# Kernel tuning notes

Hardware: AMD Instinct MI355X
Metric: run time of the kernel (lower is better)

Reference implementation:

```python
import jax, jax.numpy as jnp
import numpy as np

B, N, F, U = 4, 4096, 256, 128
NEG = -1.0e9


def setup_inputs() -> dict:
    key = jax.random.key(0)
    k1, k2, k3, k4, k5 = jax.random.split(key, 5)
    inputs = jax.random.normal(k1, (B, N, F), dtype=jnp.float32)
    # Glorot-normal-like scales
    w = jax.random.normal(k2, (F, U), dtype=jnp.float32) * np.sqrt(2.0 / (F + U)).astype(np.float32)
    ai = jax.random.normal(k3, (U, N), dtype=jnp.float32) * np.sqrt(2.0 / (U + N)).astype(np.float32)
    aj = jax.random.normal(k4, (U, N), dtype=jnp.float32) * np.sqrt(2.0 / (U + N)).astype(np.float32)
    a = (jax.random.uniform(k5, (N, N)) < 0.004).astype(jnp.float32)
    adj = jnp.maximum(a, a.T)
    return {"inputs": inputs, "w": w, "ai": ai, "aj": aj, "adj": adj}


def reference(inputs, w, ai, aj, adj):
    # f: [B, N, U]
    f = jnp.einsum('bnf,fu->bnu', inputs, w)
    # self_attn[b,i,j] = (f ai)[b,i,j]; other_attn = transpose([0,2,1]) of (f aj)
    self_attn = jnp.einsum('bnu,um->bnm', f, ai)          # [B, N, N]
    other_attn = jnp.einsum('bnu,um->bmn', f, aj)         # transposed [B, N, N]
    mask = adj + jnp.eye(N, dtype=adj.dtype)              # allow self + neighbors
    attn = self_attn + other_attn + NEG * (1.0 - mask)
    attn = jax.nn.softmax(attn, axis=1)                   # softmax over rows (axis=1)
    # out[b,j,u] = sum_i f[b,i,u] * attn[b,i,j]
    out = jnp.einsum('biu,bij->bju', f, attn)
    return jax.nn.relu(out), attn
```

## Files before the change

### kernel.cpp

```cpp
#include <hip/hip_runtime.h>
#include <hip/hip_bf16.h>

#define NN 4096
#define UU 128
#define BB 4
#define FF 256
#define MAXD 128

typedef float fv4 __attribute__((ext_vector_type(4)));

__device__ __forceinline__ unsigned short f2bf(float x) {
    unsigned int u = __float_as_uint(x);
    unsigned int r = (u + 0x7fffu + ((u >> 16) & 1u)) >> 16;
    return (unsigned short)r;
}
__device__ __forceinline__ float bf2f(unsigned short h) {
    return __uint_as_float(((unsigned int)h) << 16);
}

template <int CTRL, int RMASK>
__device__ __forceinline__ float dpp_step(float x) {
    int ti = __builtin_amdgcn_update_dpp(0, __float_as_int(x), CTRL, RMASK, 0xf, true);
    return x + __int_as_float(ti);
}
__device__ __forceinline__ float wave_sum_dpp(float x) {
    x = dpp_step<0x111, 0xf>(x);
    x = dpp_step<0x112, 0xf>(x);
    x = dpp_step<0x114, 0xf>(x);
    x = dpp_step<0x118, 0xf>(x);
    x = dpp_step<0x142, 0xa>(x);
    x = dpp_step<0x143, 0xc>(x);
    return __int_as_float(__builtin_amdgcn_readlane(__float_as_int(x), 63));
}

__global__ __launch_bounds__(256) void stage1(const float* __restrict__ A,
                                              const float* __restrict__ Wm,
                                              const float* __restrict__ adj,
                                              const float* __restrict__ ai,
                                              const float* __restrict__ aj,
                                              unsigned short* __restrict__ F,
                                              unsigned short* __restrict__ csc,
                                              int* __restrict__ cnt,
                                              int* __restrict__ dblf,
                                              unsigned short* __restrict__ aiT,
                                              unsigned short* __restrict__ ajT) {
    __shared__ __align__(16) char smem[21504];
    int t = threadIdx.x;
    int bid = blockIdx.x;

    if (bid < 512) {
        float (*As)[36]  = (float(*)[36])smem;
        float (*Ws)[132] = (float(*)[132])(smem + 4608);
        int r0 = bid * 32;
        int cg = t & 31;
        int rg = t >> 5;
        float acc[4][4] = {};
        for (int kc = 0; kc < FF; kc += 32) {
            {
                int row = t >> 3;
                int kb = (t & 7) * 4;
                const float* ap = A + (size_t)(r0 + row) * FF + kc + kb;
                float4 v0 = *(const float4*)(ap);
                As[kb + 0][row] = v0.x; As[kb + 1][row] = v0.y;
                As[kb + 2][row] = v0.z; As[kb + 3][row] = v0.w;
            }
#pragma unroll
            for (int q = 0; q < 4; q++) {
                int idx = q * 256 + t;
                int k = idx >> 5;
                int c4 = (idx & 31) * 4;
                *(float4*)&Ws[k][c4] = *(const float4*)(Wm + (size_t)(kc + k) * UU + c4);
            }
            __syncthreads();
#pragma unroll 8
            for (int kk = 0; kk < 32; kk++) {
                float4 a4 = *(const float4*)&As[kk][rg * 4];
                float4 w4 = *(const float4*)&Ws[kk][cg * 4];
                acc[0][0] += a4.x * w4.x; acc[0][1] += a4.x * w4.y; acc[0][2] += a4.x * w4.z; acc[0][3] += a4.x * w4.w;
                acc[1][0] += a4.y * w4.x; acc[1][1] += a4.y * w4.y; acc[1][2] += a4.y * w4.z; acc[1][3] += a4.y * w4.w;
                acc[2][0] += a4.z * w4.x; acc[2][1] += a4.z * w4.y; acc[2][2] += a4.z * w4.z; acc[2][3] += a4.z * w4.w;
                acc[3][0] += a4.w * w4.x; acc[3][1] += a4.w * w4.y; acc[3][2] += a4.w * w4.z; acc[3][3] += a4.w * w4.w;
            }
            __syncthreads();
        }
#pragma unroll
        for (int i = 0; i < 4; i++) {
            ushort4 h;
            h.x = f2bf(acc[i][0]); h.y = f2bf(acc[i][1]);
            h.z = f2bf(acc[i][2]); h.w = f2bf(acc[i][3]);
            *(ushort4*)(F + (size_t)(r0 + rg * 4 + i) * UU + cg * 4) = h;
        }
    } else if (bid < 4608) {
        unsigned short* tmp = (unsigned short*)smem;
        int* cd = (int*)(smem + 256);
        int j = bid - 512;
        if (t == 0) { cd[0] = 0; cd[1] = 0; }
        __syncthreads();
        const float4* row = (const float4*)(adj + (size_t)j * NN);
#pragma unroll
        for (int k = 0; k < 4; k++) {
            int q = t + k * 256;
            float4 v = row[q];
            int base = q * 4;
            float vals[4] = {v.x, v.y, v.z, v.w};
#pragma unroll
            for (int s = 0; s < 4; s++) {
                int i = base + s;
                bool nz = (vals[s] != 0.0f);
                if (i == j) { if (nz) cd[1] = 1; nz = true; }
                if (nz) {
                    int p = atomicAdd(&cd[0], 1);
                    if (p < MAXD) tmp[p] = (unsigned short)i;
                }
            }
        }
        __syncthreads();
        int M = cd[0] < MAXD ? cd[0] : MAXD;
        if (t < M) csc[(size_t)j * MAXD + t] = tmp[t];
        if (t == 0) { cnt[j] = M; dblf[j] = cd[1]; }
    } else {
        float (*tile)[33] = (float(*)[33])smem;
        int r = bid - 4608;
        int z = r >> 9;
        int rem = r & 511;
        int n0 = (rem >> 2) * 32;
        int u0 = (rem & 3) * 32;
        const float* src = z ? aj : ai;
        unsigned short* dst = z ? ajT : aiT;
        int tx = t & 31;
        int ty = t >> 5;
        for (int rr = 0; rr < 32; rr += 8)
            tile[ty + rr][tx] = src[(size_t)(u0 + ty + rr) * NN + n0 + tx];
        __syncthreads();
        for (int rr = 0; rr < 32; rr += 8)
            dst[(size_t)(n0 + ty + rr) * UU + u0 + tx] = f2bf(tile[tx][ty + rr]);
    }
}

__global__ __launch_bounds__(256) void gat_cols(const unsigned short* __restrict__ csc,
                                                const int* __restrict__ cnt,
                                                const int* __restrict__ dblf,
                                                const unsigned short* __restrict__ f,
                                                const unsigned short* __restrict__ aiT,
                                                const unsigned short* __restrict__ ajT,
                                                float* __restrict__ out,
                                                float* __restrict__ invden) {
    __shared__ unsigned short sidx[MAXD];
    int tid = threadIdx.x;
    int j = blockIdx.x;
    int lane = tid & 63, b = tid >> 6;
    int M = cnt[j];
    int oneh = dblf[j];
    if (tid < MAXD) sidx[tid] = csc[(size_t)j * MAXD + tid];

    const unsigned short* fb = f + (size_t)b * NN * UU;
    ushort2 fjh = *(const ushort2*)(fb + (size_t)j * UU + 2 * lane);
    float fjx = bf2f(fjh.x), fjy = bf2f(fjh.y);

    if (oneh) {
        float2 o;
        o.x = fjx > 0.0f ? fjx : 0.0f;
        o.y = fjy > 0.0f ? fjy : 0.0f;
        *(float2*)(out + ((size_t)(b * NN + j)) * UU + 2 * lane) = o;
        return;
    }
    __syncthreads();

    ushort2 aih = *(const ushort2*)(aiT + (size_t)j * UU + 2 * lane);
    float aix = bf2f(aih.x), aiy = bf2f(aih.y);
    float denom = 0.0f, acc0 = 0.0f, acc1 = 0.0f;

    int e = 0;
    for (; e + 2 <= M; e += 2) {
        int ia = sidx[e], ib2 = sidx[e + 1];
        ushort2 fha = *(const ushort2*)(fb + (size_t)ia * UU + 2 * lane);
        ushort2 aha = *(const ushort2*)(ajT + (size_t)ia * UU + 2 * lane);
        ushort2 fhb = *(const ushort2*)(fb + (size_t)ib2 * UU + 2 * lane);
        ushort2 ahb = *(const ushort2*)(ajT + (size_t)ib2 * UU + 2 * lane);
        float fax = bf2f(fha.x), fay = bf2f(fha.y);
        float fbx = bf2f(fhb.x), fby = bf2f(fhb.y);
        float pa = fax * aix + fay * aiy + fjx * bf2f(aha.x) + fjy * bf2f(aha.y);
        float pb = fbx * aix + fby * aiy + fjx * bf2f(ahb.x) + fjy * bf2f(ahb.y);
        float sa = wave_sum_dpp(pa);
        float sb = wave_sum_dpp(pb);
        float exa = __expf(sa);
        float exb = __expf(sb);
        denom += exa + exb;
        acc0 += exa * fax + exb * fbx;
        acc1 += exa * fay + exb * fby;
    }
    for (; e < M; e++) {
        int i = sidx[e];
        ushort2 fih = *(const ushort2*)(fb + (size_t)i * UU + 2 * lane);
        ushort2 ajh = *(const ushort2*)(ajT + (size_t)i * UU + 2 * lane);
        float fix = bf2f(fih.x), fiy = bf2f(fih.y);
        float p = fix * aix + fiy * aiy + fjx * bf2f(ajh.x) + fjy * bf2f(ajh.y);
        float ex = __expf(wave_sum_dpp(p));
        denom += ex;
        acc0 += ex * fix;
        acc1 += ex * fiy;
    }
    float inv = 1.0f / denom;

    float2 o;
    o.x = acc0 * inv; o.y = acc1 * inv;
    o.x = o.x > 0.0f ? o.x : 0.0f;
    o.y = o.y > 0.0f ? o.y : 0.0f;
    *(float2*)(out + ((size_t)(b * NN + j)) * UU + 2 * lane) = o;

    if (lane == 0) invden[(size_t)b * NN + j] = inv;
}

__global__ __launch_bounds__(256) void gat_rows(const unsigned short* __restrict__ csc,
                                                const int* __restrict__ cnt,
                                                const int* __restrict__ dblf,
                                                const unsigned short* __restrict__ f,
                                                const unsigned short* __restrict__ aiT,
                                                const unsigned short* __restrict__ ajT,
                                                const float* __restrict__ invden,
                                                float* __restrict__ attn) {
    __shared__ float rowv[NN];
    __shared__ unsigned short sidx[MAXD];
    int tid = threadIdx.x;
    int bi = blockIdx.x;
    int b = bi >> 12;
    int i = bi & (NN - 1);

    float4 z4 = {0.f, 0.f, 0.f, 0.f};
#pragma unroll
    for (int q = 0; q < 4; q++)
        *(float4*)&rowv[(q * 256 + tid) * 4] = z4;
    int M = cnt[i];
    if (tid < MAXD) sidx[tid] = csc[(size_t)i * MAXD + tid];
    __syncthreads();

    int lane = tid & 63, w = tid >> 6;
    const unsigned short* fb = f + (size_t)b * NN * UU;
    ushort2 fih = *(const ushort2*)(fb + (size_t)i * UU + 2 * lane);
    float fix_ = bf2f(fih.x), fiy_ = bf2f(fih.y);
    ushort2 ajh = *(const ushort2*)(ajT + (size_t)i * UU + 2 * lane);
    float ajx = bf2f(ajh.x), ajy = bf2f(ajh.y);

    for (int e = w; e < M; e += 4) {
        int j = sidx[e];
        float val;
        if (dblf[j]) {
            val = (i == j) ? 1.0f : 0.0f;
        } else {
            ushort2 fjh = *(const ushort2*)(fb + (size_t)j * UU + 2 * lane);
            ushort2 aih = *(const ushort2*)(aiT + (size_t)j * UU + 2 * lane);
            float p = fix_ * bf2f(aih.x) + fiy_ * bf2f(aih.y)
                    + bf2f(fjh.x) * ajx + bf2f(fjh.y) * ajy;
            float s = wave_sum_dpp(p);
            val = __expf(s) * invden[(size_t)b * NN + j];
        }
        if (lane == 0) rowv[j] = val;
    }
    __syncthreads();

    float* dst = attn + (size_t)bi * NN;
#pragma unroll
    for (int q = 0; q < 4; q++) {
        int c = (q * 256 + tid) * 4;
        fv4 v = *(fv4*)&rowv[c];
        __builtin_nontemporal_store(v, (fv4*)(dst + c));
    }
}

extern "C" void kernel_launch(void* const* d_in, const int* in_sizes, int n_in,
                              void* d_out, int out_size, void* d_ws, size_t ws_size,
                              hipStream_t stream) {
    const float* inputs = (const float*)d_in[0];
    const float* w      = (const float*)d_in[1];
    const float* ai     = (const float*)d_in[2];
    const float* aj     = (const float*)d_in[3];
    const float* adj    = (const float*)d_in[4];

    float* out  = (float*)d_out;
    float* attn = out + (size_t)BB * NN * UU;

    unsigned short* f   = (unsigned short*)d_ws;
    unsigned short* aiT = f + (size_t)BB * NN * UU;
    unsigned short* ajT = aiT + (size_t)NN * UU;
    unsigned short* csc = ajT + (size_t)NN * UU;
    int* cnt  = (int*)(csc + (size_t)NN * MAXD);
    int* dblf = cnt + NN;
    float* invden = (float*)(dblf + NN);

    stage1<<<5632, 256, 0, stream>>>(inputs, w, adj, ai, aj, f, csc, cnt, dblf, aiT, ajT);
    gat_cols<<<NN, 256, 0, stream>>>(csc, cnt, dblf, f, aiT, ajT, out, invden);
    gat_rows<<<BB * NN, 256, 0, stream>>>(csc, cnt, dblf, f, aiT, ajT, invden, attn);
}
```

Baseline: 387.7 us.

## Store per-edge attention weights in column pass and scatter them into rows

The column kernel now keeps each edge's exp value, scales it by the inverse denominator and writes it to a per-column buffer. A new set of blocks builds a row-to-(column, edge slot) map with atomics. The row kernel then just gathers these stored values instead of recomputing dot products, wave reductions and exps. This removes the duplicated score computation in exchange for extra workspace traffic and an atomic map-building step.

After: 413.3 us. +6.6%, slower.

```diff
diff --git a/kernel.cpp b/kernel.cpp
--- a/kernel.cpp
+++ b/kernel.cpp
@@ -43,7 +43,8 @@
                                               int* __restrict__ cnt,
                                               int* __restrict__ dblf,
                                               unsigned short* __restrict__ aiT,
-                                              unsigned short* __restrict__ ajT) {
+                                              unsigned short* __restrict__ ajT,
+                                              int* __restrict__ mcnt) {
     __shared__ __align__(16) char smem[21504];
     int t = threadIdx.x;
     int bid = blockIdx.x;
@@ -118,7 +119,7 @@
         int M = cd[0] < MAXD ? cd[0] : MAXD;
         if (t < M) csc[(size_t)j * MAXD + t] = tmp[t];
         if (t == 0) { cnt[j] = M; dblf[j] = cd[1]; }
-    } else {
+    } else if (bid < 5632) {
         float (*tile)[33] = (float(*)[33])smem;
         int r = bid - 4608;
         int z = r >> 9;
@@ -134,30 +135,54 @@
         __syncthreads();
         for (int rr = 0; rr < 32; rr += 8)
             dst[(size_t)(n0 + ty + rr) * UU + u0 + tx] = f2bf(tile[tx][ty + rr]);
-    }
-}
-
-__global__ __launch_bounds__(256) void gat_cols(const unsigned short* __restrict__ csc,
-                                                const int* __restrict__ cnt,
-                                                const int* __restrict__ dblf,
-                                                const unsigned short* __restrict__ f,
-                                                const unsigned short* __restrict__ aiT,
-                                                const unsigned short* __restrict__ ajT,
-                                                float* __restrict__ out,
-                                                float* __restrict__ invden) {
+    } else {
+        int4 z = {0, 0, 0, 0};
+#pragma unroll
+        for (int q = 0; q < 4; q++)
+            *(int4*)&mcnt[(q * 256 + t) * 4] = z;
+    }
+}
+
+__global__ __launch_bounds__(256) void stage2(const unsigned short* __restrict__ csc,
+                                              const int* __restrict__ cnt,
+                                              const int* __restrict__ dblf,
+                                              const unsigned short* __restrict__ f,
+                                              const unsigned short* __restrict__ aiT,
+                                              const unsigned short* __restrict__ ajT,
+                                              float* __restrict__ out,
+                                              float* __restrict__ tmpv,
+                                              unsigned int* __restrict__ mJE,
+                                              int* __restrict__ mcnt) {
+    int tid = threadIdx.x;
+    int bid = blockIdx.x;
+    int j = bid >> 1;
+
+    if (bid & 1) {
+        int M = cnt[j];
+        if (tid < M) {
+            int i = csc[(size_t)j * MAXD + tid];
+            int p = atomicAdd(&mcnt[i], 1);
+            mJE[(size_t)i * MAXD + p] = ((unsigned int)j << 7) | (unsigned int)tid;
+        }
+        return;
+    }
+
     __shared__ unsigned short sidx[MAXD];
-    int tid = threadIdx.x;
-    int j = blockIdx.x;
     int lane = tid & 63, b = tid >> 6;
     int M = cnt[j];
     int oneh = dblf[j];
     if (tid < MAXD) sidx[tid] = csc[(size_t)j * MAXD + tid];
 
     const unsigned short* fb = f + (size_t)b * NN * UU;
+    float* tv = tmpv + (((size_t)b << 12) + j) * MAXD;
     ushort2 fjh = *(const ushort2*)(fb + (size_t)j * UU + 2 * lane);
     float fjx = bf2f(fjh.x), fjy = bf2f(fjh.y);
 
     if (oneh) {
+        int g0 = csc[(size_t)j * MAXD + lane];
+        int g1 = csc[(size_t)j * MAXD + lane + 64];
+        if (lane < M)      tv[lane]      = (g0 == j) ? 1.0f : 0.0f;
+        if (lane + 64 < M) tv[lane + 64] = (g1 == j) ? 1.0f : 0.0f;
         float2 o;
         o.x = fjx > 0.0f ? fjx : 0.0f;
         o.y = fjy > 0.0f ? fjy : 0.0f;
@@ -169,6 +194,7 @@
     ushort2 aih = *(const ushort2*)(aiT + (size_t)j * UU + 2 * lane);
     float aix = bf2f(aih.x), aiy = bf2f(aih.y);
     float denom = 0.0f, acc0 = 0.0f, acc1 = 0.0f;
+    float keep0 = 0.0f, keep1 = 0.0f;
 
     int e = 0;
     for (; e + 2 <= M; e += 2) {
@@ -188,6 +214,8 @@
         denom += exa + exb;
         acc0 += exa * fax + exb * fbx;
         acc1 += exa * fay + exb * fby;
+        if ((e & 63) == lane)       { if (e < 64)     keep0 = exa; else keep1 = exa; }
+        if (((e + 1) & 63) == lane) { if (e + 1 < 64) keep0 = exb; else keep1 = exb; }
     }
     for (; e < M; e++) {
         int i = sidx[e];
@@ -199,6 +227,7 @@
         denom += ex;
         acc0 += ex * fix;
         acc1 += ex * fiy;
+        if ((e & 63) == lane) { if (e < 64) keep0 = ex; else keep1 = ex; }
     }
     float inv = 1.0f / denom;
 
@@ -208,54 +237,37 @@
     o.y = o.y > 0.0f ? o.y : 0.0f;
     *(float2*)(out + ((size_t)(b * NN + j)) * UU + 2 * lane) = o;
 
-    if (lane == 0) invden[(size_t)b * NN + j] = inv;
-}
-
-__global__ __launch_bounds__(256) void gat_rows(const unsigned short* __restrict__ csc,
-                                                const int* __restrict__ cnt,
-                                                const int* __restrict__ dblf,
-                                                const unsigned short* __restrict__ f,
-                                                const unsigned short* __restrict__ aiT,
-                                                const unsigned short* __restrict__ ajT,
-                                                const float* __restrict__ invden,
+    if (lane < M)      tv[lane]      = keep0 * inv;
+    if (lane + 64 < M) tv[lane + 64] = keep1 * inv;
+}
+
+__global__ __launch_bounds__(256) void gat_rows(const int* __restrict__ cnt,
+                                                const float* __restrict__ tmpv,
+                                                const unsigned int* __restrict__ mJE,
                                                 float* __restrict__ attn) {
     __shared__ float rowv[NN];
-    __shared__ unsigned short sidx[MAXD];
     int tid = threadIdx.x;
     int bi = blockIdx.x;
     int b = bi >> 12;
     int i = bi & (NN - 1);
 
-    float4 z4 = {0.f, 0.f, 0.f, 0.f};
+    int M = cnt[i];
+    int j = 0;
+    float val = 0.0f;
+    if (tid < M) {
+        unsigned int v = mJE[(size_t)i * MAXD + tid];
+        j = v >> 7;
+        int e = v & 127;
+        val = tmpv[(((size_t)b << 12) + j) * MAXD + e];
+    }
+
+    fv4 z = {0.f, 0.f, 0.f, 0.f};
 #pragma unroll
     for (int q = 0; q < 4; q++)
-        *(float4*)&rowv[(q * 256 + tid) * 4] = z4;
-    int M = cnt[i];
-    if (tid < MAXD) sidx[tid] = csc[(size_t)i * MAXD + tid];
+        *(fv4*)&rowv[(q * 256 + tid) * 4] = z;
     __syncthreads();
 
-    int lane = tid & 63, w = tid >> 6;
-    const unsigned short* fb = f + (size_t)b * NN * UU;
-    ushort2 fih = *(const ushort2*)(fb + (size_t)i * UU + 2 * lane);
-    float fix_ = bf2f(fih.x), fiy_ = bf2f(fih.y);
-    ushort2 ajh = *(const ushort2*)(ajT + (size_t)i * UU + 2 * lane);
-    float ajx = bf2f(ajh.x), ajy = bf2f(ajh.y);
-
-    for (int e = w; e < M; e += 4) {
-        int j = sidx[e];
-        float val;
-        if (dblf[j]) {
-            val = (i == j) ? 1.0f : 0.0f;
-        } else {
-            ushort2 fjh = *(const ushort2*)(fb + (size_t)j * UU + 2 * lane);
-            ushort2 aih = *(const ushort2*)(aiT + (size_t)j * UU + 2 * lane);
-            float p = fix_ * bf2f(aih.x) + fiy_ * bf2f(aih.y)
-                    + bf2f(fjh.x) * ajx + bf2f(fjh.y) * ajy;
-            float s = wave_sum_dpp(p);
-            val = __expf(s) * invden[(size_t)b * NN + j];
-        }
-        if (lane == 0) rowv[j] = val;
-    }
+    if (tid < M) rowv[j] = val;
     __syncthreads();
 
     float* dst = attn + (size_t)bi * NN;
@@ -285,9 +297,11 @@
     unsigned short* csc = ajT + (size_t)NN * UU;
     int* cnt  = (int*)(csc + (size_t)NN * MAXD);
     int* dblf = cnt + NN;
-    float* invden = (float*)(dblf + NN);
-
-    stage1<<<5632, 256, 0, stream>>>(inputs, w, adj, ai, aj, f, csc, cnt, dblf, aiT, ajT);
-    gat_cols<<<NN, 256, 0, stream>>>(csc, cnt, dblf, f, aiT, ajT, out, invden);
-    gat_rows<<<BB * NN, 256, 0, stream>>>(csc, cnt, dblf, f, aiT, ajT, invden, attn);
-}
+    int* mcnt = dblf + NN;
+    float* tmpv = (float*)(mcnt + NN);
+    unsigned int* mJE = (unsigned int*)(tmpv + (size_t)BB * NN * MAXD);
+
+    stage1<<<5633, 256, 0, stream>>>(inputs, w, adj, ai, aj, f, csc, cnt, dblf, aiT, ajT, mcnt);
+    stage2<<<2 * NN, 256, 0, stream>>>(csc, cnt, dblf, f, aiT, ajT, out, tmpv, mJE, mcnt);
+    gat_rows<<<BB * NN, 256, 0, stream>>>(cnt, tmpv, mJE, attn);
+}
```
